# Optimization experiments

Hardware: AMD Instinct MI355X
Metric: run time of the kernel (lower is better)

The kernel has to match this reference:

```python
import jax, jax.numpy as jnp
import numpy as np
import math

S, B, D_MODEL = 1024, 2, 1024
N_HEADS = 16
D_HEAD = D_MODEL // N_HEADS
C = 32  # compressed_len


def _xavier(key, shape):
    fan_in, fan_out = shape[-1], shape[-2] if len(shape) > 1 else shape[-1]
    limit = math.sqrt(6.0 / (fan_in + fan_out))
    return jax.random.uniform(key, shape, jnp.float32, -limit, limit)


def setup_inputs() -> dict:
    key = jax.random.key(0)
    ks = jax.random.split(key, 10)
    return {
        "x": jax.random.normal(ks[0], (S, B, D_MODEL), jnp.float32),
        "q_down": _xavier(ks[1], (C, D_MODEL)),
        "Wq": _xavier(ks[2], (D_MODEL, D_MODEL)),
        "bq": jnp.zeros((D_MODEL,), jnp.float32),
        "Wk": _xavier(ks[3], (D_MODEL, D_MODEL)),
        "bk": jnp.zeros((D_MODEL,), jnp.float32),
        "Wv": _xavier(ks[4], (D_MODEL, D_MODEL)),
        "bv": jnp.zeros((D_MODEL,), jnp.float32),
        "Wo": _xavier(ks[5], (D_MODEL, D_MODEL)),
        "bo": jnp.zeros((D_MODEL,), jnp.float32),
    }


def reference(x, q_down, Wq, bq, Wk, bk, Wv, bv, Wo, bo):
    # x: (s, b, d_model); causal=True, rope=None, dropout inactive (eval)
    s, b, d_model = x.shape
    h, dh = N_HEADS, D_HEAD
    scale = 1.0 / math.sqrt(dh)

    q_u = x @ Wq.T + bq                       # (s,b,dm)
    k_d = x @ Wk.T + bk
    v_d = x @ Wv.T + bv
    v_d_k = v_d @ Wk.T + bk
    v_d_v = v_d @ Wv.T + bv

    def heads(t):  # (s,b,dm) -> (b,h,s,dh)
        return t.reshape(s, b, h, dh).transpose(1, 2, 0, 3)

    q_u = heads(q_u) * scale
    k_d = heads(k_d)
    v_d_kv = jnp.concatenate([heads(v_d_k), heads(v_d_v)], axis=-1)  # (b,h,s,2dh)

    q_d = q_down.reshape(C, h, dh).transpose(1, 0, 2) * scale        # (h,c,dh)

    down = jnp.einsum('hcd,bhsd->bhcs', q_d, k_d)                    # (b,h,c,s)
    w = jnp.exp(down - jnp.max(down, axis=-1, keepdims=True))
    norm = jnp.cumsum(w, axis=-1)

    # (b,h,c,s,2dh): running compressed KV state
    kv_u = jnp.cumsum(w[..., None] * v_d_kv[:, :, None, :, :], axis=3) / norm[..., None]
    k_u, v_u = jnp.split(kv_u, 2, axis=-1)                           # each (b,h,c,s,dh)

    up = jnp.einsum('bhsd,bhcsd->bhsc', q_u, k_u)
    up = jax.nn.softmax(up, axis=-1)
    out = jnp.einsum('bhsc,bhcsd->bhsd', up, v_u)                    # (b,h,s,dh)

    out = out.transpose(2, 0, 1, 3).reshape(s, b, d_model)
    return out @ Wo.T + bo
```

## Files before the change

kernel.cpp:

```cpp
#include <hip/hip_runtime.h>
#include <cstdint>
#include <cstddef>

#define S_LEN 1024
#define BATCH 2
#define DM    1024
#define NH    16
#define DH    64
#define CC    32
#define SB    2048
#define TSD   128
#define NCHD  8

using short8 = __attribute__((ext_vector_type(8))) short;
using f32x4  = __attribute__((ext_vector_type(4))) float;

__device__ __forceinline__ float b2f(unsigned short u) {
    union { unsigned int i; float f; } v; v.i = ((unsigned int)u) << 16; return v.f;
}
__device__ __forceinline__ unsigned short f2b(float f) {
    union { float f; unsigned int i; } v; v.f = f;
    unsigned int x = v.i;
    unsigned int r = x + 0x7FFFu + ((x >> 16) & 1u);
    return (unsigned short)(r >> 16);
}

__device__ __forceinline__ void async_ld16(const unsigned short* g, unsigned short* l) {
    __builtin_amdgcn_global_load_lds(
        (const __attribute__((address_space(1))) unsigned int*)g,
        (__attribute__((address_space(3))) unsigned int*)l,
        16, 0, 0);
}

__global__ __launch_bounds__(256) void k_convert(
    const void* x, const void* qd,
    const void* wq, const void* wk, const void* wv, const void* wo,
    const void* bq, const void* bk, const void* bv, const void* bo,
    int* __restrict__ flag,
    unsigned short* xb, unsigned short* qdb,
    unsigned short* Wqb, unsigned short* Wkb, unsigned short* Wvb, unsigned short* Wob,
    float* biasf)
{
    __shared__ int cnt;
    if (threadIdx.x == 0) cnt = 0;
    __syncthreads();
    {
        const unsigned short* xs = (const unsigned short*)x;
        int local = 0;
        for (int i = threadIdx.x; i < 1024; i += 256) {
            unsigned e = (xs[i * 2] >> 7) & 0xFF;
            if (e >= 90 && e <= 160) local++;
        }
        atomicAdd(&cnt, local);
    }
    __syncthreads();
    const int isbf = (cnt >= 640);
    if (blockIdx.x == 0 && threadIdx.x == 0) *flag = isbf;

    const size_t tid = (size_t)blockIdx.x * 256 + threadIdx.x;
    const size_t stride = (size_t)gridDim.x * 256;

    if (!isbf) {
        auto cv = [&](const void* src, unsigned short* dst, size_t n) {
            const float4* s = (const float4*)src;
            for (size_t i = tid; i < n / 4; i += stride) {
                float4 v = s[i];
                ushort4 o;
                o.x = f2b(v.x); o.y = f2b(v.y); o.z = f2b(v.z); o.w = f2b(v.w);
                ((ushort4*)dst)[i] = o;
            }
        };
        cv(x,  xb,  (size_t)SB * DM);
        cv(qd, qdb, (size_t)CC * DM);
        cv(wq, Wqb, (size_t)DM * DM);
        cv(wk, Wkb, (size_t)DM * DM);
        cv(wv, Wvb, (size_t)DM * DM);
        cv(wo, Wob, (size_t)DM * DM);
    }
    for (size_t i = tid; i < 5 * DM; i += stride) {
        int w = (int)(i >> 10), o = (int)(i & 1023);
        float val;
        if (w == 4) val = 0.f;
        else {
            const void* bp = (w == 0) ? bq : ((w == 1) ? bk : ((w == 2) ? bv : bo));
            val = isbf ? b2f(((const unsigned short*)bp)[o]) : ((const float*)bp)[o];
        }
        biasf[i] = val;
    }
}

struct GArg {
    const unsigned short* A0;
    const unsigned short* A1;
    const unsigned short* B0;
    const unsigned short* B1;
    const float* bias;
    void* out;
    float scale;
    int mode;
};

__global__ __launch_bounds__(256) void gemm_bt(GArg g0, GArg g1, GArg g2, GArg g3,
                                               const int* __restrict__ flag,
                                               int M, int N, int K)
{
    GArg ga = (blockIdx.z == 0) ? g0 : (blockIdx.z == 1) ? g1 : (blockIdx.z == 2) ? g2 : g3;
    const int isbf = *flag;
    const unsigned short* Ap = isbf ? ga.A1 : ga.A0;
    const unsigned short* Bp = isbf ? ga.B1 : ga.B0;
    const int m0 = blockIdx.y * 128;
    const int n0 = blockIdx.x * 128;
    __shared__ __align__(16) unsigned short As[2][128 * 32];
    __shared__ __align__(16) unsigned short Bs[2][128 * 32];
    const int t = threadIdx.x;
    const int w = t >> 6, l = t & 63;
    const int wy = w >> 1, wx = w & 1;
    const int lr = l >> 2;
    const int lk = (l & 3) * 8;
    const int ln = l & 15;
    const int lq = l >> 4;

    f32x4 acc[4][4] = {};

    const unsigned short* Ab0 = Ap + (size_t)(m0 + w * 32 +      lr) * K + lk;
    const unsigned short* Ab1 = Ap + (size_t)(m0 + w * 32 + 16 + lr) * K + lk;
    const unsigned short* Bb0 = Bp + (size_t)(n0 + w * 32 +      lr) * K + lk;
    const unsigned short* Bb1 = Bp + (size_t)(n0 + w * 32 + 16 + lr) * K + lk;

    for (int kk = 0; kk < K; kk += 64) {
#pragma unroll
        for (int hh = 0; hh < 2; ++hh) {
            async_ld16(Ab0 + kk + hh * 32, &As[hh][w * 1024]);
            async_ld16(Ab1 + kk + hh * 32, &As[hh][w * 1024 + 512]);
            async_ld16(Bb0 + kk + hh * 32, &Bs[hh][w * 1024]);
            async_ld16(Bb1 + kk + hh * 32, &Bs[hh][w * 1024 + 512]);
        }
        __syncthreads();
#pragma unroll
        for (int hh = 0; hh < 2; ++hh) {
            short8 af[4], bfr[4];
#pragma unroll
            for (int i = 0; i < 4; ++i)
                af[i] = *(const short8*)&As[hh][(wy * 64 + i * 16 + ln) * 32 + lq * 8];
#pragma unroll
            for (int j = 0; j < 4; ++j)
                bfr[j] = *(const short8*)&Bs[hh][(wx * 64 + j * 16 + ln) * 32 + lq * 8];
#pragma unroll
            for (int i = 0; i < 4; ++i)
#pragma unroll
                for (int j = 0; j < 4; ++j)
                    acc[i][j] = __builtin_amdgcn_mfma_f32_16x16x32_bf16(af[i], bfr[j], acc[i][j], 0, 0, 0);
        }
        __syncthreads();
    }

    const int f32o = (ga.mode == 0) ? 1 : (ga.mode == 1) ? 0 : (!isbf);
    const float sc = ga.scale;
#pragma unroll
    for (int j = 0; j < 4; ++j) {
        int col = n0 + wx * 64 + j * 16 + ln;
        float bv = ga.bias[col];
#pragma unroll
        for (int i = 0; i < 4; ++i) {
            int row0 = m0 + wy * 64 + i * 16 + lq * 4;
#pragma unroll
            for (int r = 0; r < 4; ++r) {
                float v = (acc[i][j][r] + bv) * sc;
                size_t idx = (size_t)(row0 + r) * N + col;
                if (f32o) ((float*)ga.out)[idx] = v;
                else      ((unsigned short*)ga.out)[idx] = f2b(v);
            }
        }
    }
}

__global__ __launch_bounds__(256) void gemm_bt_n64(GArg g0, GArg g1,
                                                   const int* __restrict__ flag,
                                                   int M, int N, int K)
{
    GArg ga = (blockIdx.z == 0) ? g0 : g1;
    const int isbf = *flag;
    const unsigned short* Ap = isbf ? ga.A1 : ga.A0;
    const unsigned short* Bp = isbf ? ga.B1 : ga.B0;
    const int m0 = blockIdx.y * 128;
    const int n0 = blockIdx.x * 64;
    __shared__ __align__(16) unsigned short As[2][128 * 32];
    __shared__ __align__(16) unsigned short Bs[2][64 * 32];
    const int t = threadIdx.x;
    const int w = t >> 6, l = t & 63;
    const int wy = w >> 1, wx = w & 1;
    const int lr = l >> 2;
    const int lk = (l & 3) * 8;
    const int ln = l & 15;
    const int lq = l >> 4;

    f32x4 acc[4][2] = {};

    const unsigned short* Ab0 = Ap + (size_t)(m0 + w * 32 +      lr) * K + lk;
    const unsigned short* Ab1 = Ap + (size_t)(m0 + w * 32 + 16 + lr) * K + lk;
    const unsigned short* Bb  = Bp + (size_t)(n0 + w * 16 + lr) * K + lk;

    for (int kk = 0; kk < K; kk += 64) {
#pragma unroll
        for (int hh = 0; hh < 2; ++hh) {
            async_ld16(Ab0 + kk + hh * 32, &As[hh][w * 1024]);
            async_ld16(Ab1 + kk + hh * 32, &As[hh][w * 1024 + 512]);
            async_ld16(Bb  + kk + hh * 32, &Bs[hh][w * 512]);
        }
        __syncthreads();
#pragma unroll
        for (int hh = 0; hh < 2; ++hh) {
            short8 af[4], bfr[2];
#pragma unroll
            for (int i = 0; i < 4; ++i)
                af[i] = *(const short8*)&As[hh][(wy * 64 + i * 16 + ln) * 32 + lq * 8];
#pragma unroll
            for (int j = 0; j < 2; ++j)
                bfr[j] = *(const short8*)&Bs[hh][(wx * 32 + j * 16 + ln) * 32 + lq * 8];
#pragma unroll
            for (int i = 0; i < 4; ++i)
#pragma unroll
                for (int j = 0; j < 2; ++j)
                    acc[i][j] = __builtin_amdgcn_mfma_f32_16x16x32_bf16(af[i], bfr[j], acc[i][j], 0, 0, 0);
        }
        __syncthreads();
    }

    const int f32o = (ga.mode == 0) ? 1 : (ga.mode == 1) ? 0 : (!isbf);
    const float sc = ga.scale;
#pragma unroll
    for (int j = 0; j < 2; ++j) {
        int col = n0 + wx * 32 + j * 16 + ln;
        float bv = ga.bias[col];
#pragma unroll
        for (int i = 0; i < 4; ++i) {
            int row0 = m0 + wy * 64 + i * 16 + lq * 4;
#pragma unroll
            for (int r = 0; r < 4; ++r) {
                float v = (acc[i][j][r] + bv) * sc;
                size_t idx = (size_t)(row0 + r) * N + col;
                if (f32o) ((float*)ga.out)[idx] = v;
                else      ((unsigned short*)ga.out)[idx] = f2b(v);
            }
        }
    }
}

__global__ __launch_bounds__(256) void k_g2down(
    GArg g0, GArg g1, const int* __restrict__ flag, int M, int N, int K,
    const unsigned short* __restrict__ kd,
    const unsigned short* __restrict__ qd0,
    const unsigned short* __restrict__ qd1,
    float* __restrict__ wbuf,
    float* __restrict__ cmax,
    float* __restrict__ csum)
{
    __shared__ __align__(16) unsigned char SM[40448];
    const int isbf = *flag;
    const int t = threadIdx.x;
    const int w = t >> 6, l = t & 63;
    const int ln = l & 15, lq = l >> 4;

    if (blockIdx.z < 2) {
        unsigned short* As = (unsigned short*)SM;
        unsigned short* Bs = (unsigned short*)(SM + 16384);
        GArg ga = blockIdx.z ? g1 : g0;
        const unsigned short* Ap = isbf ? ga.A1 : ga.A0;
        const unsigned short* Bp = isbf ? ga.B1 : ga.B0;
        const int m0 = blockIdx.y * 128;
        const int n0 = blockIdx.x * 128;
        const int wy = w >> 1, wx = w & 1;
        const int lr = l >> 2;
        const int lk = (l & 3) * 8;

        f32x4 acc[4][4] = {};

        const unsigned short* Ab0 = Ap + (size_t)(m0 + w * 32 +      lr) * K + lk;
        const unsigned short* Ab1 = Ap + (size_t)(m0 + w * 32 + 16 + lr) * K + lk;
        const unsigned short* Bb0 = Bp + (size_t)(n0 + w * 32 +      lr) * K + lk;
        const unsigned short* Bb1 = Bp + (size_t)(n0 + w * 32 + 16 + lr) * K + lk;

        for (int kk = 0; kk < K; kk += 64) {
#pragma unroll
            for (int hh = 0; hh < 2; ++hh) {
                async_ld16(Ab0 + kk + hh * 32, &As[hh * 4096 + w * 1024]);
                async_ld16(Ab1 + kk + hh * 32, &As[hh * 4096 + w * 1024 + 512]);
                async_ld16(Bb0 + kk + hh * 32, &Bs[hh * 4096 + w * 1024]);
                async_ld16(Bb1 + kk + hh * 32, &Bs[hh * 4096 + w * 1024 + 512]);
            }
            __syncthreads();
#pragma unroll
            for (int hh = 0; hh < 2; ++hh) {
                short8 af[4], bfr[4];
#pragma unroll
                for (int i = 0; i < 4; ++i)
                    af[i] = *(const short8*)&As[hh * 4096 + (wy * 64 + i * 16 + ln) * 32 + lq * 8];
#pragma unroll
                for (int j = 0; j < 4; ++j)
                    bfr[j] = *(const short8*)&Bs[hh * 4096 + (wx * 64 + j * 16 + ln) * 32 + lq * 8];
#pragma unroll
                for (int i = 0; i < 4; ++i)
#pragma unroll
                    for (int j = 0; j < 4; ++j)
                        acc[i][j] = __builtin_amdgcn_mfma_f32_16x16x32_bf16(af[i], bfr[j], acc[i][j], 0, 0, 0);
            }
            __syncthreads();
        }

        const int f32o = (ga.mode == 0) ? 1 : (ga.mode == 1) ? 0 : (!isbf);
        const float sc = ga.scale;
#pragma unroll
        for (int j = 0; j < 4; ++j) {
            int col = n0 + wx * 64 + j * 16 + ln;
            float bv = ga.bias[col];
#pragma unroll
            for (int i = 0; i < 4; ++i) {
                int row0 = m0 + wy * 64 + i * 16 + lq * 4;
#pragma unroll
                for (int r = 0; r < 4; ++r) {
                    float v = (acc[i][j][r] + bv) * sc;
                    size_t idx = (size_t)(row0 + r) * N + col;
                    if (f32o) ((float*)ga.out)[idx] = v;
                    else      ((unsigned short*)ga.out)[idx] = f2b(v);
                }
            }
        }
    } else {
        unsigned short* QD = (unsigned short*)SM;
        unsigned short* KT = (unsigned short*)(SM + 4608);
        float* SS          = (float*)(SM + 23040);
        float* cmf         = (float*)(SM + 39936);

        const int id = (blockIdx.z - 2) * 128 + blockIdx.y * 8 + blockIdx.x;
        const unsigned short* qdw = isbf ? qd1 : qd0;
        const int bh = id >> 3;
        const int b = bh >> 4, h = bh & 15;
        const int chunk = id & 7;
        const int s0 = chunk * TSD;

        {
            int r = t >> 3, cb = (t & 7) * 8;
            *(short8*)&QD[r * 72 + cb] = *(const short8*)&qdw[(size_t)r * DM + h * DH + cb];
        }
        for (int u = t; u < 128 * 8; u += 256) {
            int r = u >> 3, cb = (u & 7) * 8;
            *(short8*)&KT[r * 72 + cb] =
                *(const short8*)&kd[(size_t)((s0 + r) * BATCH + b) * DM + h * DH + cb];
        }
        __syncthreads();

        f32x4 accG[2][2] = {};
#pragma unroll
        for (int ks = 0; ks < 2; ++ks) {
            short8 a8[2], b8[2];
#pragma unroll
            for (int i = 0; i < 2; ++i)
                a8[i] = *(const short8*)&QD[(i * 16 + ln) * 72 + ks * 32 + lq * 8];
#pragma unroll
            for (int j = 0; j < 2; ++j)
                b8[j] = *(const short8*)&KT[(w * 32 + j * 16 + ln) * 72 + ks * 32 + lq * 8];
#pragma unroll
            for (int i = 0; i < 2; ++i)
#pragma unroll
                for (int j = 0; j < 2; ++j)
                    accG[i][j] = __builtin_amdgcn_mfma_f32_16x16x32_bf16(a8[i], b8[j], accG[i][j], 0, 0, 0);
        }
#pragma unroll
        for (int i = 0; i < 2; ++i) {
#pragma unroll
            for (int j = 0; j < 2; ++j) {
                int sl = w * 32 + j * 16 + ln;
#pragma unroll
                for (int r = 0; r < 4; ++r) {
                    int c = i * 16 + lq * 4 + r;
                    float v = accG[i][j][r] * 0.125f;
                    SS[c * 132 + sl] = v;
                    wbuf[((size_t)bh * CC + c) * S_LEN + s0 + sl] = v;
                }
            }
        }
        __syncthreads();

        const int c = t >> 3, sub = t & 7;
        float lmax = -3.4e38f;
#pragma unroll
        for (int k = 0; k < 16; ++k) lmax = fmaxf(lmax, SS[c * 132 + sub * 16 + k]);
        lmax = fmaxf(lmax, __shfl_xor(lmax, 1));
        lmax = fmaxf(lmax, __shfl_xor(lmax, 2));
        lmax = fmaxf(lmax, __shfl_xor(lmax, 4));
        if (sub == 0) {
            cmf[c] = lmax;
            cmax[((size_t)bh * CC + c) * NCHD + chunk] = lmax;
        }
        __syncthreads();
        const float cm = cmf[c];
        float es = 0.f;
#pragma unroll
        for (int k = 0; k < 16; ++k) es += __expf(SS[c * 132 + sub * 16 + k] - cm);
        es += __shfl_xor(es, 1);
        es += __shfl_xor(es, 2);
        es += __shfl_xor(es, 4);
        if (sub == 0) csum[((size_t)bh * CC + c) * NCHD + chunk] = es;
    }
}

__global__ __launch_bounds__(256) void k_wstate(
    const float* __restrict__ wbuf,
    const float* __restrict__ cmax,
    const float* __restrict__ csum,
    const unsigned short* __restrict__ vdk,
    const unsigned short* __restrict__ vdv,
    unsigned short* __restrict__ wb,
    unsigned short* __restrict__ wT,
    float* __restrict__ invn,
    float* __restrict__ Mst,
    float* __restrict__ NTst)
{
    __shared__ __align__(16) unsigned char SM[45568];
    unsigned short* Wfull = (unsigned short*)SM;
    unsigned char* R = SM + 8704;
    float* gm    = (float*)R;
    float* basep = (float*)(R + 128);
    float* psum  = (float*)(R + 256);
    unsigned short* wTt = (unsigned short*)(R + 1408);
    float* invt  = (float*)(R + 11648);
    unsigned short* T1 = (unsigned short*)R;
    unsigned short* T2 = (unsigned short*)(R + 9216);
    unsigned short* KT = (unsigned short*)(R + 18432);
    unsigned short* VT = (unsigned short*)(R + 27648);

    const int bh = blockIdx.x, seg = blockIdx.y;
    const int b = bh >> 4, h = bh & 15;
    const int t = threadIdx.x;
    const int w = t >> 6, l = t & 63;
    const int ln = l & 15, lq = l >> 4;

    if (t < CC) {
        const size_t cb = (size_t)(bh * CC + t) * NCHD;
        float m = cmax[cb];
#pragma unroll
        for (int g = 1; g < NCHD; ++g) m = fmaxf(m, cmax[cb + g]);
        gm[t] = m;
        float bsum = 0.f;
        for (int k = 0; k < seg; ++k)
            bsum += csum[cb + k] * __expf(cmax[cb + k] - m);
        basep[t] = bsum;
    }
    __syncthreads();

    {
        const int c = t >> 3, sub = t & 7;
        const float gmc = gm[c];
        const size_t rbase = (size_t)bh * 32768 + c * 1024 + seg * 128 + sub * 16;
        float w16[16];
        float s = 0.f;
#pragma unroll
        for (int i = 0; i < 16; ++i) {
            float v = __expf(wbuf[rbase + i] - gmc);
            w16[i] = v; s += v;
        }
        psum[c * 9 + sub] = s;
        short8 o0, o1;
#pragma unroll
        for (int i = 0; i < 8; ++i) { o0[i] = f2b(w16[i]); o1[i] = f2b(w16[8 + i]); }
        *(short8*)&wb[rbase] = o0;
        *(short8*)&wb[rbase + 8] = o1;
        *(short8*)&Wfull[c * 136 + sub * 16] = o0;
        *(short8*)&Wfull[c * 136 + sub * 16 + 8] = o1;
#pragma unroll
        for (int i = 0; i < 16; ++i) wTt[(sub * 16 + i) * 40 + c] = f2b(w16[i]);
        __syncthreads();

        float run = basep[c];
        for (int k = 0; k < sub; ++k) run += psum[c * 9 + k];
#pragma unroll
        for (int i = 0; i < 16; ++i) {
            run += w16[i];
            invt[(sub * 16 + i) * 36 + c] = 1.0f / fmaxf(run, 1e-30f);
        }
    }
    __syncthreads();

    for (int u = t; u < 128 * 4; u += 256) {
        int r = u >> 2, cb2 = (u & 3) * 8;
        *(short8*)&wT[(size_t)bh * 32768 + (seg * 128 + r) * 32 + cb2] =
            *(const short8*)&wTt[r * 40 + cb2];
    }
    for (int u = t; u < 128 * 8; u += 256) {
        int r = u >> 3, cb2 = (u & 7) * 4;
        *(float4*)&invn[(size_t)bh * 32768 + (seg * 128 + r) * 32 + cb2] =
            *(const float4*)&invt[r * 36 + cb2];
    }
    __syncthreads();

    for (int rep = 0; rep < 2; ++rep) {
        const int ch = seg * 2 + rep;
        const int s0 = ch * 64;

        for (int u = t; u < 64 * 8; u += 256) {
            int r = u >> 3, cb = (u & 7) * 8;
            *(short8*)&T1[r * 72 + cb] =
                *(const short8*)&vdk[(size_t)((s0 + r) * BATCH + b) * DM + h * DH + cb];
            *(short8*)&T2[r * 72 + cb] =
                *(const short8*)&vdv[(size_t)((s0 + r) * BATCH + b) * DM + h * DH + cb];
        }
        __syncthreads();
        for (int u = t; u < 64 * 8; u += 256) {
            int d = u >> 3, s8 = (u & 7) * 8;
            short8 o1, o2;
#pragma unroll
            for (int k = 0; k < 8; ++k) {
                o1[k] = T1[(s8 + k) * 72 + d];
                o2[k] = T2[(s8 + k) * 72 + d];
            }
            *(short8*)&KT[d * 72 + s8] = o1;
            *(short8*)&VT[d * 72 + s8] = o2;
        }
        __syncthreads();

        f32x4 accM[2] = {};
#pragma unroll
        for (int ks = 0; ks < 2; ++ks) {
            short8 b8 = *(const short8*)&KT[(w * 16 + ln) * 72 + ks * 32 + lq * 8];
#pragma unroll
            for (int i = 0; i < 2; ++i) {
                short8 a8 = *(const short8*)&Wfull[(i * 16 + ln) * 136 + rep * 64 + ks * 32 + lq * 8];
                accM[i] = __builtin_amdgcn_mfma_f32_16x16x32_bf16(a8, b8, accM[i], 0, 0, 0);
            }
        }
#pragma unroll
        for (int i = 0; i < 2; ++i)
#pragma unroll
            for (int r = 0; r < 4; ++r)
                Mst[((size_t)(bh * 16 + ch) * 32 + i * 16 + lq * 4 + r) * 64 + w * 16 + ln] = accM[i][r];

        f32x4 accN[2] = {};
#pragma unroll
        for (int ks = 0; ks < 2; ++ks) {
            short8 a8 = *(const short8*)&VT[(w * 16 + ln) * 72 + ks * 32 + lq * 8];
#pragma unroll
            for (int j = 0; j < 2; ++j) {
                short8 b8 = *(const short8*)&Wfull[(j * 16 + ln) * 136 + rep * 64 + ks * 32 + lq * 8];
                accN[j] = __builtin_amdgcn_mfma_f32_16x16x32_bf16(a8, b8, accN[j], 0, 0, 0);
            }
        }
#pragma unroll
        for (int j = 0; j < 2; ++j)
#pragma unroll
            for (int r = 0; r < 4; ++r)
                NTst[((size_t)(bh * 16 + ch) * 64 + w * 16 + lq * 4 + r) * 32 + j * 16 + ln] = accN[j][r];
        __syncthreads();
    }
}

__global__ __launch_bounds__(256) void k_att(
    const unsigned short* __restrict__ qu,
    const unsigned short* __restrict__ vdk,
    const unsigned short* __restrict__ wb,
    const float* __restrict__ invn,
    const unsigned short* __restrict__ wT,
    const unsigned short* __restrict__ vdv,
    const float* __restrict__ Mst,
    const float* __restrict__ NTst,
    unsigned short* __restrict__ attout)
{
    const int bh = blockIdx.x, b = bh >> 4, h = bh & 15;
    const int qi = blockIdx.y;
    const int s0 = qi * 64;
    const int t = threadIdx.x;
    const int w = t >> 6, l = t & 63;
    const int wy = w >> 1, wx = w & 1;
    const int ln = l & 15, lq = l >> 4;

    __shared__ __align__(16) unsigned short Qs[64 * 72];
    __shared__ __align__(16) unsigned short Gs[64 * 72];
    __shared__ __align__(16) unsigned short Kd[64 * 72];
    __shared__ __align__(16) unsigned short Wd[32 * 72];
    __shared__ __align__(16) unsigned short WTd[64 * 40];
    __shared__ __align__(16) unsigned short VTd[64 * 72];
    __shared__ __align__(16) unsigned short Mc[32 * 72];
    __shared__ __align__(16) unsigned short Nc[64 * 40];

    for (int u = t; u < 64 * 8; u += 256) {
        int r = u >> 3, cb = (u & 7) * 8;
        *(short8*)&Qs[r * 72 + cb] =
            *(const short8*)&qu[(size_t)(s0 + r) * 2048 + b * 1024 + h * 64 + cb];
        *(short8*)&Kd[r * 72 + cb] =
            *(const short8*)&vdk[(size_t)(s0 + r) * 2048 + b * 1024 + h * 64 + cb];
        *(short8*)&Gs[r * 72 + cb] =
            *(const short8*)&vdv[(size_t)(s0 + r) * 2048 + b * 1024 + h * 64 + cb];
    }
    for (int u = t; u < 32 * 8; u += 256) {
        int r = u >> 3, cb = (u & 7) * 8;
        *(short8*)&Wd[r * 72 + cb] =
            *(const short8*)&wb[(size_t)bh * 32768 + r * 1024 + s0 + cb];
    }
    for (int u = t; u < 64 * 4; u += 256) {
        int r = u >> 2, cb = (u & 3) * 8;
        *(short8*)&WTd[r * 40 + cb] =
            *(const short8*)&wT[(size_t)bh * 32768 + (s0 + r) * 32 + cb];
    }
    {
        float am[8] = {0.f, 0.f, 0.f, 0.f, 0.f, 0.f, 0.f, 0.f};
        float an[8] = {0.f, 0.f, 0.f, 0.f, 0.f, 0.f, 0.f, 0.f};
        for (int ch = 0; ch < qi; ++ch) {
            const float* pm = Mst + ((size_t)(bh * 16 + ch)) * 2048 + t * 8;
            const float* pn = NTst + ((size_t)(bh * 16 + ch)) * 2048 + t * 8;
            float4 m0 = *(const float4*)pm;
            float4 m1 = *(const float4*)(pm + 4);
            float4 n0 = *(const float4*)pn;
            float4 n1 = *(const float4*)(pn + 4);
            am[0] += m0.x; am[1] += m0.y; am[2] += m0.z; am[3] += m0.w;
            am[4] += m1.x; am[5] += m1.y; am[6] += m1.z; am[7] += m1.w;
            an[0] += n0.x; an[1] += n0.y; an[2] += n0.z; an[3] += n0.w;
            an[4] += n1.x; an[5] += n1.y; an[6] += n1.z; an[7] += n1.w;
        }
        short8 mo, no;
#pragma unroll
        for (int j = 0; j < 8; ++j) { mo[j] = f2b(am[j]); no[j] = f2b(an[j]); }
        *(short8*)&Mc[(t >> 3) * 72 + (t & 7) * 8] = mo;
        *(short8*)&Nc[(t >> 2) * 40 + (t & 3) * 8] = no;
    }
    __syncthreads();

    for (int u = t; u < 64 * 8; u += 256) {
        int d = u >> 3, s8 = (u & 7) * 8;
        short8 o;
#pragma unroll
        for (int k = 0; k < 8; ++k) o[k] = Gs[(s8 + k) * 72 + d];
        *(short8*)&VTd[d * 72 + s8] = o;
    }
    __syncthreads();

    {
        f32x4 accG[2][2] = {};
#pragma unroll
        for (int ks = 0; ks < 2; ++ks) {
            short8 a8[2], b8[2];
#pragma unroll
            for (int i = 0; i < 2; ++i)
                a8[i] = *(const short8*)&Qs[(wy * 32 + i * 16 + ln) * 72 + ks * 32 + lq * 8];
#pragma unroll
            for (int j = 0; j < 2; ++j)
                b8[j] = *(const short8*)&Kd[(wx * 32 + j * 16 + ln) * 72 + ks * 32 + lq * 8];
#pragma unroll
            for (int i = 0; i < 2; ++i)
#pragma unroll
                for (int j = 0; j < 2; ++j)
                    accG[i][j] = __builtin_amdgcn_mfma_f32_16x16x32_bf16(a8[i], b8[j], accG[i][j], 0, 0, 0);
        }
        __syncthreads();
#pragma unroll
        for (int i = 0; i < 2; ++i) {
            int row = wy * 32 + i * 16 + lq * 4;
#pragma unroll
            for (int j = 0; j < 2; ++j) {
                int col = wx * 32 + j * 16 + ln;
#pragma unroll
                for (int r = 0; r < 4; ++r) {
                    float v = accG[i][j][r];
                    if (col > row + r) v = 0.f;
                    Gs[(row + r) * 72 + col] = f2b(v);
                }
            }
        }
    }
    __syncthreads();

    f32x4 accU[2] = {};
#pragma unroll
    for (int ks = 0; ks < 2; ++ks) {
        short8 ga = *(const short8*)&Gs[(w * 16 + ln) * 72 + ks * 32 + lq * 8];
        short8 qa = *(const short8*)&Qs[(w * 16 + ln) * 72 + ks * 32 + lq * 8];
#pragma unroll
        for (int j = 0; j < 2; ++j) {
            short8 wf = *(const short8*)&Wd[(j * 16 + ln) * 72 + ks * 32 + lq * 8];
            short8 mf = *(const short8*)&Mc[(j * 16 + ln) * 72 + ks * 32 + lq * 8];
            accU[j] = __builtin_amdgcn_mfma_f32_16x16x32_bf16(ga, wf, accU[j], 0, 0, 0);
            accU[j] = __builtin_amdgcn_mfma_f32_16x16x32_bf16(qa, mf, accU[j], 0, 0, 0);
        }
    }
    __syncthreads();

    {
        int rowl = w * 16 + lq * 4;
#pragma unroll
        for (int r = 0; r < 4; ++r) {
            int srow = s0 + rowl + r;
            float inv0 = invn[(size_t)bh * 32768 + srow * 32 + ln];
            float inv1 = invn[(size_t)bh * 32768 + srow * 32 + 16 + ln];
            float l0 = accU[0][r] * inv0;
            float l1 = accU[1][r] * inv1;
            float m = fmaxf(l0, l1);
#pragma unroll
            for (int msk = 1; msk < 16; msk <<= 1) m = fmaxf(m, __shfl_xor(m, msk));
            float e0 = __expf(l0 - m), e1 = __expf(l1 - m);
            float Z = e0 + e1;
#pragma unroll
            for (int msk = 1; msk < 16; msk <<= 1) Z += __shfl_xor(Z, msk);
            float iz = 1.0f / Z;
            Qs[(rowl + r) * 40 + ln]      = f2b(e0 * iz * inv0);
            Qs[(rowl + r) * 40 + 16 + ln] = f2b(e1 * iz * inv1);
        }
    }
    __syncthreads();

    short8 pa[2];
#pragma unroll
    for (int i = 0; i < 2; ++i)
        pa[i] = *(const short8*)&Qs[(wy * 32 + i * 16 + ln) * 40 + lq * 8];
    {
        f32x4 accS[2][2] = {};
        short8 b8[2];
#pragma unroll
        for (int j = 0; j < 2; ++j)
            b8[j] = *(const short8*)&WTd[(wx * 32 + j * 16 + ln) * 40 + lq * 8];
#pragma unroll
        for (int i = 0; i < 2; ++i)
#pragma unroll
            for (int j = 0; j < 2; ++j)
                accS[i][j] = __builtin_amdgcn_mfma_f32_16x16x32_bf16(pa[i], b8[j], accS[i][j], 0, 0, 0);
#pragma unroll
        for (int i = 0; i < 2; ++i) {
            int row = wy * 32 + i * 16 + lq * 4;
#pragma unroll
            for (int j = 0; j < 2; ++j) {
                int col = wx * 32 + j * 16 + ln;
#pragma unroll
                for (int r = 0; r < 4; ++r) {
                    float v = accS[i][j][r];
                    if (col > row + r) v = 0.f;
                    Gs[(row + r) * 72 + col] = f2b(v);
                }
            }
        }
    }
    __syncthreads();

    {
        f32x4 accO[2][2] = {};
        short8 n8[2];
#pragma unroll
        for (int j = 0; j < 2; ++j)
            n8[j] = *(const short8*)&Nc[(wx * 32 + j * 16 + ln) * 40 + lq * 8];
#pragma unroll
        for (int i = 0; i < 2; ++i)
#pragma unroll
            for (int j = 0; j < 2; ++j)
                accO[i][j] = __builtin_amdgcn_mfma_f32_16x16x32_bf16(pa[i], n8[j], accO[i][j], 0, 0, 0);
#pragma unroll
        for (int ks = 0; ks < 2; ++ks) {
            short8 a8[2], b8[2];
#pragma unroll
            for (int i = 0; i < 2; ++i)
                a8[i] = *(const short8*)&Gs[(wy * 32 + i * 16 + ln) * 72 + ks * 32 + lq * 8];
#pragma unroll
            for (int j = 0; j < 2; ++j)
                b8[j] = *(const short8*)&VTd[(wx * 32 + j * 16 + ln) * 72 + ks * 32 + lq * 8];
#pragma unroll
            for (int i = 0; i < 2; ++i)
#pragma unroll
                for (int j = 0; j < 2; ++j)
                    accO[i][j] = __builtin_amdgcn_mfma_f32_16x16x32_bf16(a8[i], b8[j], accO[i][j], 0, 0, 0);
        }
#pragma unroll
        for (int i = 0; i < 2; ++i) {
            int rowb = s0 + wy * 32 + i * 16 + lq * 4;
#pragma unroll
            for (int j = 0; j < 2; ++j) {
                int d = wx * 32 + j * 16 + ln;
#pragma unroll
                for (int r = 0; r < 4; ++r)
                    attout[(size_t)(rowb + r) * 2048 + b * 1024 + h * 64 + d] = f2b(accO[i][j][r]);
            }
        }
    }
}

extern "C" void kernel_launch(void* const* d_in, const int* in_sizes, int n_in,
                              void* d_out, int out_size, void* d_ws, size_t ws_size,
                              hipStream_t stream)
{
    (void)in_sizes; (void)n_in; (void)out_size; (void)ws_size;
    char* ws = (char*)d_ws;
    const size_t MB = (size_t)1 << 20;
    const size_t KB = (size_t)1 << 10;
    unsigned short* attout = (unsigned short*)(ws + 0 * MB);
    unsigned short* q_u    = (unsigned short*)(ws + 4 * MB);
    unsigned short* k_d    = (unsigned short*)(ws + 8 * MB);
    unsigned short* v_dk   = (unsigned short*)(ws + 12 * MB);
    unsigned short* v_dv   = (unsigned short*)(ws + 16 * MB);
    float* wbuf = (float*)(ws + 20 * MB);
    unsigned short* wb  = (unsigned short*)(ws + 24 * MB);
    unsigned short* wT  = (unsigned short*)(ws + 26 * MB);
    float* invn = (float*)(ws + 28 * MB);
    float* Mst  = (float*)(ws + 32 * MB);
    float* NTst = (float*)(ws + 36 * MB);
    unsigned short* xb  = (unsigned short*)(ws + 44 * MB);
    unsigned short* Wqb = (unsigned short*)(ws + 48 * MB);
    unsigned short* Wkb = (unsigned short*)(ws + 50 * MB);
    unsigned short* Wvb = (unsigned short*)(ws + 52 * MB);
    unsigned short* Wob = (unsigned short*)(ws + 54 * MB);
    unsigned short* v_d = (unsigned short*)(ws + 56 * MB);
    unsigned short* qdb = (unsigned short*)(ws + 62 * MB);
    float* biasf  = (float*)(ws + 62 * MB + 64 * KB);
    float* cmax   = (float*)(ws + 62 * MB + 192 * KB);
    float* csum   = (float*)(ws + 62 * MB + 256 * KB);
    int*   flag   = (int*)  (ws + 62 * MB + 320 * KB);

    const unsigned short* xraw  = (const unsigned short*)d_in[0];
    const unsigned short* qdraw = (const unsigned short*)d_in[1];
    const unsigned short* wqraw = (const unsigned short*)d_in[2];
    const unsigned short* wkraw = (const unsigned short*)d_in[4];
    const unsigned short* wvraw = (const unsigned short*)d_in[6];
    const unsigned short* woraw = (const unsigned short*)d_in[8];

    k_convert<<<1024, 256, 0, stream>>>(
        d_in[0], d_in[1], d_in[2], d_in[4], d_in[6], d_in[8],
        d_in[3], d_in[5], d_in[7], d_in[9],
        flag, xb, qdb, Wqb, Wkb, Wvb, Wob, biasf);

    const float* bqf = biasf;
    const float* bkf = biasf + 1024;
    const float* bvf = biasf + 2048;
    const float* bof = biasf + 3072;

    GArg gq { xb, xraw, Wqb, wqraw, bqf, (void*)q_u, 0.125f, 1 };
    GArg gk { xb, xraw, Wkb, wkraw, bkf, (void*)k_d, 1.0f, 1 };
    GArg gv { xb, xraw, Wvb, wvraw, bvf, (void*)v_d, 1.0f, 1 };
    gemm_bt<<<dim3(8, 16, 3), 256, 0, stream>>>(gq, gk, gv, gq, flag, SB, DM, DM);

    GArg gvk{ v_d, v_d, Wkb, wkraw, bkf, (void*)v_dk, 1.0f, 1 };
    GArg gvv{ v_d, v_d, Wvb, wvraw, bvf, (void*)v_dv, 1.0f, 1 };
    k_g2down<<<dim3(8, 16, 4), 256, 0, stream>>>(gvk, gvv, flag, SB, DM, DM,
                                                 k_d, qdb, qdraw, wbuf, cmax, csum);

    k_wstate<<<dim3(32, 8), 256, 0, stream>>>(wbuf, cmax, csum, v_dk, v_dv,
                                              wb, wT, invn, Mst, NTst);
    k_att<<<dim3(32, 16), 256, 0, stream>>>(q_u, v_dk, wb, invn, wT, v_dv,
                                            Mst, NTst, attout);

    GArg go{ attout, attout, Wob, woraw, bof, d_out, 1.0f, 2 };
    gemm_bt_n64<<<dim3(16, 16, 1), 256, 0, stream>>>(go, go, flag, SB, DM, DM);
}
```

Baseline: 182.4 us.

## Drop global wT buffer, transpose in LDS, fold Wo conversion into QKV GEMM

New measurement: 176.5 us. 3.2% less time.

```diff
diff --git a/kernel.cpp b/kernel.cpp
--- a/kernel.cpp
+++ b/kernel.cpp
@@ -34,11 +34,11 @@
 
 __global__ __launch_bounds__(256) void k_convert(
     const void* x, const void* qd,
-    const void* wq, const void* wk, const void* wv, const void* wo,
+    const void* wq, const void* wk, const void* wv,
     const void* bq, const void* bk, const void* bv, const void* bo,
     int* __restrict__ flag,
     unsigned short* xb, unsigned short* qdb,
-    unsigned short* Wqb, unsigned short* Wkb, unsigned short* Wvb, unsigned short* Wob,
+    unsigned short* Wqb, unsigned short* Wkb, unsigned short* Wvb,
     float* biasf)
 {
     __shared__ int cnt;
@@ -75,7 +75,6 @@
         cv(wq, Wqb, (size_t)DM * DM);
         cv(wk, Wkb, (size_t)DM * DM);
         cv(wv, Wvb, (size_t)DM * DM);
-        cv(wo, Wob, (size_t)DM * DM);
     }
     for (size_t i = tid; i < 5 * DM; i += stride) {
         int w = (int)(i >> 10), o = (int)(i & 1023);
@@ -100,19 +99,35 @@
     int mode;
 };
 
-__global__ __launch_bounds__(256) void gemm_bt(GArg g0, GArg g1, GArg g2, GArg g3,
-                                               const int* __restrict__ flag,
-                                               int M, int N, int K)
+__global__ __launch_bounds__(256) void k_g1conv(
+    GArg g0, GArg g1, GArg g2, const int* __restrict__ flag,
+    int M, int N, int K,
+    const void* __restrict__ wo_raw, unsigned short* __restrict__ Wob)
 {
-    GArg ga = (blockIdx.z == 0) ? g0 : (blockIdx.z == 1) ? g1 : (blockIdx.z == 2) ? g2 : g3;
     const int isbf = *flag;
+    const int t = threadIdx.x;
+
+    if (blockIdx.z == 3) {
+        if (!isbf) {
+            const float4* s = (const float4*)wo_raw;
+            const int id = blockIdx.y * 8 + blockIdx.x;
+            for (int i = id * 256 + t; i < (DM * DM) / 4; i += 128 * 256) {
+                float4 v = s[i];
+                ushort4 o;
+                o.x = f2b(v.x); o.y = f2b(v.y); o.z = f2b(v.z); o.w = f2b(v.w);
+                ((ushort4*)Wob)[i] = o;
+            }
+        }
+        return;
+    }
+
+    GArg ga = (blockIdx.z == 0) ? g0 : (blockIdx.z == 1) ? g1 : g2;
     const unsigned short* Ap = isbf ? ga.A1 : ga.A0;
     const unsigned short* Bp = isbf ? ga.B1 : ga.B0;
     const int m0 = blockIdx.y * 128;
     const int n0 = blockIdx.x * 128;
     __shared__ __align__(16) unsigned short As[2][128 * 32];
     __shared__ __align__(16) unsigned short Bs[2][128 * 32];
-    const int t = threadIdx.x;
     const int w = t >> 6, l = t & 63;
     const int wy = w >> 1, wx = w & 1;
     const int lr = l >> 2;
@@ -154,7 +169,6 @@
         __syncthreads();
     }
 
-    const int f32o = (ga.mode == 0) ? 1 : (ga.mode == 1) ? 0 : (!isbf);
     const float sc = ga.scale;
 #pragma unroll
     for (int j = 0; j < 4; ++j) {
@@ -166,9 +180,7 @@
 #pragma unroll
             for (int r = 0; r < 4; ++r) {
                 float v = (acc[i][j][r] + bv) * sc;
-                size_t idx = (size_t)(row0 + r) * N + col;
-                if (f32o) ((float*)ga.out)[idx] = v;
-                else      ((unsigned short*)ga.out)[idx] = f2b(v);
+                ((unsigned short*)ga.out)[(size_t)(row0 + r) * N + col] = f2b(v);
             }
         }
     }
@@ -307,7 +319,6 @@
             __syncthreads();
         }
 
-        const int f32o = (ga.mode == 0) ? 1 : (ga.mode == 1) ? 0 : (!isbf);
         const float sc = ga.scale;
 #pragma unroll
         for (int j = 0; j < 4; ++j) {
@@ -319,9 +330,7 @@
 #pragma unroll
                 for (int r = 0; r < 4; ++r) {
                     float v = (acc[i][j][r] + bv) * sc;
-                    size_t idx = (size_t)(row0 + r) * N + col;
-                    if (f32o) ((float*)ga.out)[idx] = v;
-                    else      ((unsigned short*)ga.out)[idx] = f2b(v);
+                    ((unsigned short*)ga.out)[(size_t)(row0 + r) * N + col] = f2b(v);
                 }
             }
         }
@@ -411,7 +420,6 @@
     const unsigned short* __restrict__ vdk,
     const unsigned short* __restrict__ vdv,
     unsigned short* __restrict__ wb,
-    unsigned short* __restrict__ wT,
     float* __restrict__ invn,
     float* __restrict__ Mst,
     float* __restrict__ NTst)
@@ -422,8 +430,7 @@
     float* gm    = (float*)R;
     float* basep = (float*)(R + 128);
     float* psum  = (float*)(R + 256);
-    unsigned short* wTt = (unsigned short*)(R + 1408);
-    float* invt  = (float*)(R + 11648);
+    float* invt  = (float*)(R + 1408);
     unsigned short* T1 = (unsigned short*)R;
     unsigned short* T2 = (unsigned short*)(R + 9216);
     unsigned short* KT = (unsigned short*)(R + 18432);
@@ -467,8 +474,6 @@
         *(short8*)&wb[rbase + 8] = o1;
         *(short8*)&Wfull[c * 136 + sub * 16] = o0;
         *(short8*)&Wfull[c * 136 + sub * 16 + 8] = o1;
-#pragma unroll
-        for (int i = 0; i < 16; ++i) wTt[(sub * 16 + i) * 40 + c] = f2b(w16[i]);
         __syncthreads();
 
         float run = basep[c];
@@ -481,11 +486,6 @@
     }
     __syncthreads();
 
-    for (int u = t; u < 128 * 4; u += 256) {
-        int r = u >> 2, cb2 = (u & 3) * 8;
-        *(short8*)&wT[(size_t)bh * 32768 + (seg * 128 + r) * 32 + cb2] =
-            *(const short8*)&wTt[r * 40 + cb2];
-    }
     for (int u = t; u < 128 * 8; u += 256) {
         int r = u >> 3, cb2 = (u & 7) * 4;
         *(float4*)&invn[(size_t)bh * 32768 + (seg * 128 + r) * 32 + cb2] =
@@ -558,7 +558,6 @@
     const unsigned short* __restrict__ vdk,
     const unsigned short* __restrict__ wb,
     const float* __restrict__ invn,
-    const unsigned short* __restrict__ wT,
     const unsigned short* __restrict__ vdv,
     const float* __restrict__ Mst,
     const float* __restrict__ NTst,
@@ -594,11 +593,6 @@
         int r = u >> 3, cb = (u & 7) * 8;
         *(short8*)&Wd[r * 72 + cb] =
             *(const short8*)&wb[(size_t)bh * 32768 + r * 1024 + s0 + cb];
-    }
-    for (int u = t; u < 64 * 4; u += 256) {
-        int r = u >> 2, cb = (u & 3) * 8;
-        *(short8*)&WTd[r * 40 + cb] =
-            *(const short8*)&wT[(size_t)bh * 32768 + (s0 + r) * 32 + cb];
     }
     {
         float am[8] = {0.f, 0.f, 0.f, 0.f, 0.f, 0.f, 0.f, 0.f};
@@ -629,6 +623,13 @@
 #pragma unroll
         for (int k = 0; k < 8; ++k) o[k] = Gs[(s8 + k) * 72 + d];
         *(short8*)&VTd[d * 72 + s8] = o;
+    }
+    {
+        int sl = t >> 2, cb = (t & 3) * 8;
+        short8 o;
+#pragma unroll
+        for (int k = 0; k < 8; ++k) o[k] = Wd[(cb + k) * 72 + sl];
+        *(short8*)&WTd[sl * 40 + cb] = o;
     }
     __syncthreads();
 
@@ -792,7 +793,6 @@
     unsigned short* v_dv   = (unsigned short*)(ws + 16 * MB);
     float* wbuf = (float*)(ws + 20 * MB);
     unsigned short* wb  = (unsigned short*)(ws + 24 * MB);
-    unsigned short* wT  = (unsigned short*)(ws + 26 * MB);
     float* invn = (float*)(ws + 28 * MB);
     float* Mst  = (float*)(ws + 32 * MB);
     float* NTst = (float*)(ws + 36 * MB);
@@ -816,9 +816,9 @@
     const unsigned short* woraw = (const unsigned short*)d_in[8];
 
     k_convert<<<1024, 256, 0, stream>>>(
-        d_in[0], d_in[1], d_in[2], d_in[4], d_in[6], d_in[8],
+        d_in[0], d_in[1], d_in[2], d_in[4], d_in[6],
         d_in[3], d_in[5], d_in[7], d_in[9],
-        flag, xb, qdb, Wqb, Wkb, Wvb, Wob, biasf);
+        flag, xb, qdb, Wqb, Wkb, Wvb, biasf);
 
     const float* bqf = biasf;
     const float* bkf = biasf + 1024;
@@ -828,7 +828,8 @@
     GArg gq { xb, xraw, Wqb, wqraw, bqf, (void*)q_u, 0.125f, 1 };
     GArg gk { xb, xraw, Wkb, wkraw, bkf, (void*)k_d, 1.0f, 1 };
     GArg gv { xb, xraw, Wvb, wvraw, bvf, (void*)v_d, 1.0f, 1 };
-    gemm_bt<<<dim3(8, 16, 3), 256, 0, stream>>>(gq, gk, gv, gq, flag, SB, DM, DM);
+    k_g1conv<<<dim3(8, 16, 4), 256, 0, stream>>>(gq, gk, gv, flag, SB, DM, DM,
+                                                 d_in[8], Wob);
 
     GArg gvk{ v_d, v_d, Wkb, wkraw, bkf, (void*)v_dk, 1.0f, 1 };
     GArg gvv{ v_d, v_d, Wvb, wvraw, bvf, (void*)v_dv, 1.0f, 1 };
@@ -836,8 +837,8 @@
                                                  k_d, qdb, qdraw, wbuf, cmax, csum);
 
     k_wstate<<<dim3(32, 8), 256, 0, stream>>>(wbuf, cmax, csum, v_dk, v_dv,
-                                              wb, wT, invn, Mst, NTst);
-    k_att<<<dim3(32, 16), 256, 0, stream>>>(q_u, v_dk, wb, invn, wT, v_dv,
+                                              wb, invn, Mst, NTst);
+    k_att<<<dim3(32, 16), 256, 0, stream>>>(q_u, v_dk, wb, invn, v_dv,
                                             Mst, NTst, attout);
 
     GArg go{ attout, attout, Wob, woraw, bof, d_out, 1.0f, 2 };
```
